# Kernel optimization log

Hardware: AMD Instinct MI355X
Metric: run time of the kernel (lower is better)

The kernel has to match this reference:

```python
import jax, jax.numpy as jnp
import numpy as np

B, H, D = 2, 16, 64
M = N = 4096
WM = WN = 64
R = 3
NEG = -10000.0


def _rand_blocks(m, n, wm, wn, r, last_idx):
    # Faithful port of bigbird_block_rand_mask (numpy RNG, seeded by caller).
    nb = m // wm
    rand = np.zeros((nb - 2, r), dtype=np.int32)
    mid = np.arange(1, n // wn - 1, dtype=np.int32)
    last = n // wn - 1
    if last_idx > 2 * wn:
        last = last_idx // wn - 1
    for i in range(1, nb - 1):
        start, end = i - 2, i
        if i == 1:
            rand[i - 1] = np.random.permutation(mid[2:last])[:r]
        elif i == 2:
            rand[i - 1] = np.random.permutation(mid[3:last])[:r]
        elif i == nb - 3 or i == nb - 2:
            rand[i - 1] = np.random.permutation(mid[:last])[:r]
        elif start > last:
            rand[i - 1] = np.random.permutation(mid[:last])[:r]
        elif end + 1 == last:
            rand[i - 1] = np.random.permutation(mid[:start])[:r]
        else:
            rand[i - 1] = np.random.permutation(np.concatenate((mid[:start], mid[end + 1:last])))[:r]
    return rand


def setup_inputs() -> dict:
    key = jax.random.key(0)
    kq, kk, kv = jax.random.split(key, 3)
    nb = M // WM
    q = jax.random.normal(kq, (B, H, M, D), jnp.float32)
    k = jax.random.normal(kk, (B, H, N, D), jnp.float32)
    v = jax.random.normal(kv, (B, H, N, D), jnp.float32)
    band_mask = jnp.ones((B, 1, nb - 4, WM, 3 * WN), jnp.float32)
    from_mask = jnp.ones((B, 1, M, 1), jnp.float32)
    to_mask = jnp.ones((B, 1, 1, N), jnp.float32)
    from_blocked_mask = jnp.ones((B, nb, WM), jnp.float32)
    to_blocked_mask = jnp.ones((B, nb, WN), jnp.float32)
    np.random.seed(0)
    ra = np.stack([_rand_blocks(M, N, WM, WN, R, 1024)[:nb - 2] for _ in range(H)], 0)
    rand_attn = jnp.asarray(np.broadcast_to(ra[None], (B, H, nb - 2, R)).copy(), jnp.int32)
    return dict(query_layer=q, key_layer=k, value_layer=v, band_mask=band_mask,
                from_mask=from_mask, to_mask=to_mask,
                from_blocked_mask=from_blocked_mask, to_blocked_mask=to_blocked_mask,
                rand_attn=rand_attn, batch_size=B, from_seq_length=M, to_seq_length=N)


def _forward(q, k, v, band_mask, from_mask, to_mask, from_blocked_mask, to_blocked_mask, rand_attn):
    b, h, m, d = q.shape
    n = k.shape[2]
    wm, wn, r = WM, WN, R
    nb = m // wm
    scale = 1.0 / np.sqrt(d)
    bq = q.reshape(b, h, nb, wm, d)
    bk = k.reshape(b, h, nb, wn, d)
    bv = v.reshape(b, h, nb, wn, d)

    # gather random key/value blocks: [b,h,nb-2,r*wn,d]
    idx = jnp.broadcast_to(rand_attn.reshape(b, h, (nb - 2) * r, 1, 1).astype(jnp.int32),
                           (b, h, (nb - 2) * r, wn, d))
    gk = jnp.take_along_axis(bk, idx, axis=2).reshape(b, h, nb - 2, r * wn, d)
    gv = jnp.take_along_axis(bv, idx, axis=2).reshape(b, h, nb - 2, r * wn, d)

    # random-block attention mask: [b,h,nb-2,wm,r*wn]
    bidx = jnp.arange(b)[:, None, None, None]
    rm = to_blocked_mask[bidx, rand_attn].reshape(b, h, nb - 2, r * wn)
    rand_mask = jnp.einsum('blq,bhlk->bhlqk', from_blocked_mask[:, 1:-1], rm)

    # --- first row-block: full attention over all keys ---
    p0 = jnp.einsum('bhqd,bhkd->bhqk', bq[:, :, 0], k) * scale + (1.0 - to_mask) * NEG
    c0 = jnp.einsum('bhqk,bhkd->bhqd', jax.nn.softmax(p0, -1), v)[:, :, None]

    # --- second row-block: blocks 0,1,2,last + random ---
    k1c = jnp.concatenate([bk[:, :, 0], bk[:, :, 1], bk[:, :, 2], bk[:, :, -1], gk[:, :, 0]], axis=2)
    v1c = jnp.concatenate([bv[:, :, 0], bv[:, :, 1], bv[:, :, 2], bv[:, :, -1], gv[:, :, 0]], axis=2)
    p1 = jnp.einsum('bhqd,bhkd->bhqk', bq[:, :, 1], k1c) * scale
    seq_pad = jnp.concatenate([to_mask[:, :, :, :3 * wn], to_mask[:, :, :, -wn:],
                               jnp.ones((b, 1, 1, r * wn), to_mask.dtype)], axis=3)
    rpad = jnp.concatenate([jnp.ones((b, h, wm, 4 * wn), rand_mask.dtype), rand_mask[:, :, 0]], axis=3)
    p1 = p1 + (1.0 - jnp.minimum(seq_pad, rpad)) * NEG
    c1 = jnp.einsum('bhqk,bhkd->bhqd', jax.nn.softmax(p1, -1), v1c)[:, :, None]

    # --- middle row-blocks: sliding window (3 blocks) + first + last + random ---
    ek = jnp.concatenate([bk[:, :, 1:-3], bk[:, :, 2:-2], bk[:, :, 3:-1]], axis=3)  # [b,h,nb-4,3wn,d]
    ev = jnp.concatenate([bv[:, :, 1:-3], bv[:, :, 2:-2], bv[:, :, 3:-1]], axis=3)
    mq = bq[:, :, 2:-2]
    inner = jnp.einsum('bhlqd,bhlkd->bhlqk', mq, ek) * scale + (1.0 - band_mask) * NEG
    randp = jnp.einsum('bhlqd,bhlkd->bhlqk', mq, gk[:, :, 1:-1]) * scale + (1.0 - rand_mask[:, :, 1:-1]) * NEG
    firstp = jnp.einsum('bhlqd,bhkd->bhlqk', mq, bk[:, :, 0]) * scale \
        + (1.0 - to_mask[:, :, :, :wn][:, :, :, None, :]) * NEG
    lastp = jnp.einsum('bhlqd,bhkd->bhlqk', mq, bk[:, :, -1]) * scale \
        + (1.0 - to_mask[:, :, :, -wn:][:, :, :, None, :]) * NEG
    band = jnp.concatenate([firstp, inner, randp, lastp], axis=-1)  # [b,h,nb-4,wm,(5+r)*wn]
    attn = jax.nn.softmax(band, -1)
    cmid = (jnp.einsum('bhlqk,bhlkd->bhlqd', attn[..., wn:4 * wn], ev)
            + jnp.einsum('bhlqk,bhlkd->bhlqd', attn[..., 4 * wn:4 * wn + r * wn], gv[:, :, 1:-1])
            + jnp.einsum('bhlqk,bhkd->bhlqd', attn[..., :wn], bv[:, :, 0])
            + jnp.einsum('bhlqk,bhkd->bhlqd', attn[..., -wn:], bv[:, :, -1]))

    # --- second-to-last row-block: blocks 0,-3,-2,-1 + random ---
    k2c = jnp.concatenate([bk[:, :, 0], bk[:, :, -3], bk[:, :, -2], bk[:, :, -1], gk[:, :, -1]], axis=2)
    v2c = jnp.concatenate([bv[:, :, 0], bv[:, :, -3], bv[:, :, -2], bv[:, :, -1], gv[:, :, -1]], axis=2)
    p2 = jnp.einsum('bhqd,bhkd->bhqk', bq[:, :, -2], k2c) * scale
    seq_pad2 = jnp.concatenate([to_mask[:, :, :, :wn], to_mask[:, :, :, -3 * wn:],
                                jnp.ones((b, 1, 1, r * wn), to_mask.dtype)], axis=3)
    rpad2 = jnp.concatenate([jnp.ones((b, h, wm, 4 * wn), rand_mask.dtype), rand_mask[:, :, -1]], axis=3)
    p2 = p2 + (1.0 - jnp.minimum(seq_pad2, rpad2)) * NEG
    c2 = jnp.einsum('bhqk,bhkd->bhqd', jax.nn.softmax(p2, -1), v2c)[:, :, None]

    # --- last row-block: full attention ---
    p3 = jnp.einsum('bhqd,bhkd->bhqk', bq[:, :, -1], k) * scale + (1.0 - to_mask) * NEG
    c3 = jnp.einsum('bhqk,bhkd->bhqd', jax.nn.softmax(p3, -1), v)[:, :, None]

    ctx = jnp.concatenate([c0, c1, cmid, c2, c3], axis=2).reshape(b, h, m, d) * from_mask
    return jnp.transpose(ctx, (0, 2, 1, 3))  # [b, m, h, d]


def reference(query_layer, key_layer, value_layer, band_mask, from_mask, to_mask,
              from_blocked_mask, to_blocked_mask, rand_attn,
              batch_size, from_seq_length, to_seq_length):
    return _forward(query_layer, key_layer, value_layer, band_mask, from_mask, to_mask,
                    from_blocked_mask, to_blocked_mask, rand_attn)
```

## Files before the change

### kernel.cpp

```cpp
#include <hip/hip_runtime.h>
#include <math.h>

constexpr int B_  = 2;
constexpr int H_  = 16;
constexpr int M_  = 4096;
constexpr int NB_ = 64;
constexpr int R_  = 3;
constexpr float LOG2E  = 1.44269504089f;
constexpr float SCALE2 = 0.125f * LOG2E;
constexpr float NEG2   = -10000.0f * LOG2E;

constexpr int PER_BH = 62 + 16;
constexpr int NWG    = B_ * H_ * PER_BH;
constexpr int PACC_OFF = 0;
constexpr int PM_OFF   = B_ * H_ * 2 * 8 * 64 * 64;
constexpr int PL_OFF   = PM_OFF + B_ * H_ * 2 * 8 * 64;
constexpr size_t KV_BYTE_OFF = (size_t)(PL_OFF + B_ * H_ * 2 * 8 * 64) * 4;
constexpr size_t KV_BYTES    = (size_t)B_ * H_ * 64 * 1024 * 16;
constexpr size_t WS_NEED     = KV_BYTE_OFF + KV_BYTES;

constexpr int PER_BH1 = 312;
constexpr int NWG1    = B_ * H_ * PER_BH1;

typedef short bf16x8 __attribute__((ext_vector_type(8)));
typedef float f32x4  __attribute__((ext_vector_type(4)));

__device__ __forceinline__ short bf16s(float x) {
    return __builtin_bit_cast(short, (__bf16)x);
}
__device__ __forceinline__ unsigned pack_bf16(float a, float b) {
    unsigned short ul = __builtin_bit_cast(unsigned short, (__bf16)a);
    unsigned short uh = __builtin_bit_cast(unsigned short, (__bf16)b);
    return (unsigned)ul | ((unsigned)uh << 16);
}

__device__ __forceinline__ int tile_kb(int e, int ch, int qb, int ra0, int ra1, int ra2, int i) {
    if (e >= 0) return ch * 8 + i;
    const int rnd = (i == 4) ? ra0 : ((i == 5) ? ra1 : ra2);
    if (qb == 1)        return (i < 3) ? i : ((i == 3) ? NB_ - 1 : rnd);
    if (qb == NB_ - 2)  return (i == 0) ? 0 : ((i < 4) ? 60 + i : rnd);
    if (i == 0) return 0;
    if (i < 4)  return qb - 2 + i;
    if (i < 7)  return rnd;
    return NB_ - 1;
}

__device__ __forceinline__ int tile_mode(int e, int qb, int i, int& boff) {
    boff = 0;
    if (e >= 0) return 0;
    if (qb == 1 || qb == NB_ - 2) return (i >= 4) ? 2 : 0;
    if (i >= 1 && i < 4) { boff = (i - 1) * 64; return 1; }
    if (i >= 4 && i < 7) return 2;
    return 0;
}

__global__ __launch_bounds__(256)
void bigbird_prep(const float* __restrict__ k, const float* __restrict__ v,
                  int4* __restrict__ wskv)
{
    __shared__ float kt[64][66];
    __shared__ float vt[64][66];
    const int g = blockIdx.x;
    const int t = threadIdx.x;
    const int row = t >> 2, cc = (t & 3) * 16;
    const float* kp = k + (size_t)g * 4096 + row * 64 + cc;
    const float* vp = v + (size_t)g * 4096 + row * 64 + cc;
    #pragma unroll
    for (int j4 = 0; j4 < 4; ++j4) {
        *(float4*)&kt[row][cc + j4 * 4] = *(const float4*)(kp + j4 * 4);
        *(float4*)&vt[row][cc + j4 * 4] = *(const float4*)(vp + j4 * 4);
    }
    __syncthreads();
    #pragma unroll
    for (int cpt = 0; cpt < 4; ++cpt) {
        const int ch = t + cpt * 256;
        const int slot = ch >> 6, lane = ch & 63;
        bf16x8 o;
        if (slot < 8) {
            const int r  = 16 * (slot >> 1) + (lane & 15);
            const int c0 = 32 * (slot & 1) + 8 * (lane >> 4);
            #pragma unroll
            for (int j = 0; j < 8; ++j) o[j] = bf16s(kt[r][c0 + j]);
        } else {
            const int s2 = slot - 8;
            const int r0 = 32 * (s2 & 1) + 8 * (lane >> 4);
            const int c  = 16 * (s2 >> 1) + (lane & 15);
            #pragma unroll
            for (int j = 0; j < 8; ++j) o[j] = bf16s(vt[r0 + j][c]);
        }
        wskv[(size_t)g * 1024 + ch] = __builtin_bit_cast(int4, o);
    }
}

__global__ __launch_bounds__(64, 3)
void bigbird_1w(const float* __restrict__ q, const int4* __restrict__ wskv,
                const float* __restrict__ band_mask, const float* __restrict__ from_mask,
                const float* __restrict__ to_mask,   const float* __restrict__ from_blocked,
                const float* __restrict__ to_blocked, const int* __restrict__ rand_attn,
                float* __restrict__ out, float* __restrict__ ws)
{
    const int wg   = (blockIdx.x & 7) * (NWG1 / 8) + (blockIdx.x >> 3);
    const int bh   = wg / PER_BH1;
    const int idx  = wg % PER_BH1;
    const int item = idx >> 2;
    const int strip= idx & 3;
    const int h    = bh % H_;
    const int b    = bh / H_;
    int qb, e = -1, ch = 0;
    if (item < 62)      { qb = item + 1; }
    else if (item < 70) { e = 0; ch = item - 62; qb = 0; }
    else                { e = 1; ch = item - 70; qb = NB_ - 1; }

    const int l  = threadIdx.x;
    const int c  = l & 15;
    const int hh = l >> 4;

    int ra0 = 0, ra1 = 0, ra2 = 0;
    int nkb;
    if (e >= 0) nkb = 8;
    else {
        const int* ra = rand_attn + ((b * H_ + h) * (NB_ - 2) + (qb - 1)) * R_;
        ra0 = ra[0]; ra1 = ra[1]; ra2 = ra[2];
        nkb = (qb == 1 || qb == NB_ - 2) ? 7 : 8;
    }

    bf16x8 qf[2];
    {
        const float* qp = q + ((size_t)bh * M_ + (size_t)qb * 64 + strip * 16 + c) * 64 + hh * 8;
        #pragma unroll
        for (int dh = 0; dh < 2; ++dh) {
            float4 a0 = *(const float4*)(qp + dh * 32);
            float4 a1 = *(const float4*)(qp + dh * 32 + 4);
            bf16x8 qv;
            qv[0] = bf16s(a0.x); qv[1] = bf16s(a0.y); qv[2] = bf16s(a0.z); qv[3] = bf16s(a0.w);
            qv[4] = bf16s(a1.x); qv[5] = bf16s(a1.y); qv[6] = bf16s(a1.z); qv[7] = bf16s(a1.w);
            qf[dh] = qv;
        }
    }

    const float fbv = from_blocked[(b * NB_ + qb) * 64 + (strip * 16 + c)];

    float mrun = -INFINITY, lrun = 0.0f;
    f32x4 O[4];
    #pragma unroll
    for (int nf = 0; nf < 4; ++nf) { O[nf][0] = 0.f; O[nf][1] = 0.f; O[nf][2] = 0.f; O[nf][3] = 0.f; }

    for (int it = 0; it < nkb; ++it) {
        const int kb = tile_kb(e, ch, qb, ra0, ra1, ra2, it);
        int boffC; const int modeC = tile_mode(e, qb, it, boffC);
        const int4* tb = wskv + (size_t)(bh * 64 + kb) * 1024;

        int4 kfr[8];
        #pragma unroll
        for (int s = 0; s < 8; ++s) kfr[s] = tb[s * 64 + l];
        int4 vfr[8];
        #pragma unroll
        for (int s = 0; s < 8; ++s) vfr[s] = tb[(8 + s) * 64 + l];

        float msk[4][4];
        if (modeC == 0) {
            const float* mp = to_mask + b * M_ + kb * 64 + 4 * hh;
            #pragma unroll
            for (int f = 0; f < 4; ++f) {
                float4 mv = *(const float4*)(mp + 16 * f);
                msk[f][0] = mv.x; msk[f][1] = mv.y; msk[f][2] = mv.z; msk[f][3] = mv.w;
            }
        } else if (modeC == 1) {
            const float* mp = band_mask + (((size_t)b * (NB_ - 4) + (qb - 2)) * 64 + (strip * 16 + c)) * 192 + boffC + 4 * hh;
            #pragma unroll
            for (int f = 0; f < 4; ++f) {
                float4 mv = *(const float4*)(mp + 16 * f);
                msk[f][0] = mv.x; msk[f][1] = mv.y; msk[f][2] = mv.z; msk[f][3] = mv.w;
            }
        } else {
            const float* mp = to_blocked + (b * NB_ + kb) * 64 + 4 * hh;
            #pragma unroll
            for (int f = 0; f < 4; ++f) {
                float4 mv = *(const float4*)(mp + 16 * f);
                msk[f][0] = fbv * mv.x; msk[f][1] = fbv * mv.y;
                msk[f][2] = fbv * mv.z; msk[f][3] = fbv * mv.w;
            }
        }

        f32x4 sf[4];
        #pragma unroll
        for (int f = 0; f < 4; ++f) { sf[f][0]=0.f; sf[f][1]=0.f; sf[f][2]=0.f; sf[f][3]=0.f; }
        __builtin_amdgcn_s_setprio(1);
        #pragma unroll
        for (int f = 0; f < 4; ++f) {
            sf[f] = __builtin_amdgcn_mfma_f32_16x16x32_bf16(
                        __builtin_bit_cast(bf16x8, kfr[f * 2 + 0]), qf[0], sf[f], 0, 0, 0);
            sf[f] = __builtin_amdgcn_mfma_f32_16x16x32_bf16(
                        __builtin_bit_cast(bf16x8, kfr[f * 2 + 1]), qf[1], sf[f], 0, 0, 0);
        }
        __builtin_amdgcn_s_setprio(0);

        float p[4][4];
        float tmax = -INFINITY;
        #pragma unroll
        for (int f = 0; f < 4; ++f) {
            #pragma unroll
            for (int r = 0; r < 4; ++r) {
                const float s = sf[f][r] * SCALE2 + (1.0f - msk[f][r]) * NEG2;
                p[f][r] = s;
                tmax = fmaxf(tmax, s);
            }
        }
        tmax = fmaxf(tmax, __shfl_xor(tmax, 16));
        tmax = fmaxf(tmax, __shfl_xor(tmax, 32));
        const float mnew = fmaxf(mrun, tmax);
        const float fs = exp2f(mrun - mnew);
        float sum = 0.0f;
        #pragma unroll
        for (int f = 0; f < 4; ++f) {
            #pragma unroll
            for (int r = 0; r < 4; ++r) { p[f][r] = exp2f(p[f][r] - mnew); sum += p[f][r]; }
        }
        sum += __shfl_xor(sum, 16);
        sum += __shfl_xor(sum, 32);
        lrun = lrun * fs + sum;
        mrun = mnew;

        const float fr0 = __shfl(fs, hh * 4 + 0);
        const float fr1 = __shfl(fs, hh * 4 + 1);
        const float fr2 = __shfl(fs, hh * 4 + 2);
        const float fr3 = __shfl(fs, hh * 4 + 3);
        #pragma unroll
        for (int nf = 0; nf < 4; ++nf) {
            O[nf][0] *= fr0; O[nf][1] *= fr1; O[nf][2] *= fr2; O[nf][3] *= fr3;
        }

        unsigned pks[4][2];
        #pragma unroll
        for (int f = 0; f < 4; ++f) {
            pks[f][0] = pack_bf16(p[f][0], p[f][1]);
            pks[f][1] = pack_bf16(p[f][2], p[f][3]);
        }
        #pragma unroll
        for (int kh = 0; kh < 2; ++kh) {
            unsigned ad[4];
            #pragma unroll
            for (int wq = 0; wq < 4; ++wq) {
                const int pos = wq >> 1, ww = wq & 1;
                const int src = c + 16 * ((2 * hh + pos) & 3);
                const unsigned x = (unsigned)__shfl((int)pks[2 * kh][ww], src);
                const unsigned y = (unsigned)__shfl((int)pks[2 * kh + 1][ww], src);
                ad[wq] = (hh & 2) ? y : x;
            }
            const uint4 adv = make_uint4(ad[0], ad[1], ad[2], ad[3]);
            const bf16x8 pa = __builtin_bit_cast(bf16x8, adv);
            __builtin_amdgcn_s_setprio(1);
            #pragma unroll
            for (int nf = 0; nf < 4; ++nf) {
                O[nf] = __builtin_amdgcn_mfma_f32_16x16x32_bf16(
                            pa, __builtin_bit_cast(bf16x8, vfr[nf * 2 + kh]), O[nf], 0, 0, 0);
            }
            __builtin_amdgcn_s_setprio(0);
        }
    }

    if (e < 0) {
        #pragma unroll
        for (int r = 0; r < 4; ++r) {
            const float lr  = __shfl(lrun, hh * 4 + r);
            const int   qg  = qb * 64 + strip * 16 + hh * 4 + r;
            const float fmv = from_mask[b * M_ + qg];
            const float scl = fmv / lr;
            float* op = out + (((size_t)b * M_ + qg) * H_ + h) * 64 + c;
            #pragma unroll
            for (int nf = 0; nf < 4; ++nf) op[nf * 16] = O[nf][r] * scl;
        }
    } else {
        const int pe = (bh * 2 + e) * 8 + ch;
        #pragma unroll
        for (int r = 0; r < 4; ++r) {
            const int qlocal = strip * 16 + hh * 4 + r;
            float* pa = ws + PACC_OFF + ((size_t)pe * 64 + qlocal) * 64 + c;
            #pragma unroll
            for (int nf = 0; nf < 4; ++nf) pa[nf * 16] = O[nf][r];
        }
        if (hh == 0) {
            ws[PM_OFF + pe * 64 + strip * 16 + c] = mrun;
            ws[PL_OFF + pe * 64 + strip * 16 + c] = lrun;
        }
    }
}

__global__ __launch_bounds__(256, 4)
void bigbird_mfma(const float* __restrict__ q,  const float* __restrict__ k,
                  const float* __restrict__ v,  const float* __restrict__ band_mask,
                  const float* __restrict__ from_mask, const float* __restrict__ to_mask,
                  const float* __restrict__ from_blocked, const float* __restrict__ to_blocked,
                  const int*   __restrict__ rand_attn,   float* __restrict__ out,
                  float* __restrict__ ws)
{
    __shared__ int4 kf[2][8][64];
    __shared__ int4 vf[2][8][64];

    const int wg  = (blockIdx.x & 7) * (NWG / 8) + (blockIdx.x >> 3);
    const int bh  = wg / PER_BH;
    const int idx = wg % PER_BH;
    const int h   = bh % H_;
    const int b   = bh / H_;
    int qb, e = -1, ch = 0;
    if (idx < 62)      { qb = idx + 1; }
    else if (idx < 70) { e = 0; ch = idx - 62; qb = 0; }
    else               { e = 1; ch = idx - 70; qb = NB_ - 1; }

    const int t  = threadIdx.x;
    const int l  = t & 63;
    const int w  = t >> 6;
    const int c  = l & 15;
    const int hh = l >> 4;

    int ra0 = 0, ra1 = 0, ra2 = 0;
    int nkb;
    if (e >= 0) nkb = 8;
    else {
        const int* ra = rand_attn + ((b * H_ + h) * (NB_ - 2) + (qb - 1)) * R_;
        ra0 = ra[0]; ra1 = ra[1]; ra2 = ra[2];
        nkb = (qb == 1 || qb == NB_ - 2) ? 7 : 8;
    }

    const int rr  = t >> 2;
    const int cc4 = t & 3;
    const float* kbase = k + ((size_t)bh * M_ + rr) * 64 + cc4 * 16;
    const int kslot = (rr >> 4) * 2 + (cc4 >> 1);
    const int kr15  = rr & 15;
    const int kg0   = (cc4 & 1) * 2;

    const int d0v  = (t & 31) * 2;
    const int oct8 = t >> 5;
    const float* vbase = v + (size_t)bh * M_ * 64 + (size_t)(oct8 * 8) * 64 + d0v;
    const int vslot = (d0v >> 4) * 2 + (oct8 >> 2);
    const int vidx  = (oct8 & 3) * 16 + (d0v & 15);

    bf16x8 qf[2];
    {
        const float* qp = q + ((size_t)bh * M_ + (size_t)qb * 64 + w * 16 + c) * 64 + hh * 8;
        #pragma unroll
        for (int dh = 0; dh < 2; ++dh) {
            float4 a0 = *(const float4*)(qp + dh * 32);
            float4 a1 = *(const float4*)(qp + dh * 32 + 4);
            bf16x8 qv;
            qv[0] = bf16s(a0.x); qv[1] = bf16s(a0.y); qv[2] = bf16s(a0.z); qv[3] = bf16s(a0.w);
            qv[4] = bf16s(a1.x); qv[5] = bf16s(a1.y); qv[6] = bf16s(a1.z); qv[7] = bf16s(a1.w);
            qf[dh] = qv;
        }
    }

    const float fbv = from_blocked[(b * NB_ + qb) * 64 + (w * 16 + c)];

    float mrun = -INFINITY, lrun = 0.0f;
    f32x4 O[4];
    #pragma unroll
    for (int nf = 0; nf < 4; ++nf) { O[nf][0] = 0.f; O[nf][1] = 0.f; O[nf][2] = 0.f; O[nf][3] = 0.f; }

    float4 kr0, kr1, kr2, kr3;
    float2 vr[8];

    {
        const int kb0 = tile_kb(e, ch, qb, ra0, ra1, ra2, 0);
        const float4* kp4 = (const float4*)(kbase + (size_t)kb0 * 4096);
        kr0 = kp4[0]; kr1 = kp4[1]; kr2 = kp4[2]; kr3 = kp4[3];
        const float* vp = vbase + (size_t)kb0 * 4096;
        #pragma unroll
        for (int j = 0; j < 8; ++j) vr[j] = *(const float2*)(vp + j * 64);

        float kfl[16];
        kfl[0]=kr0.x; kfl[1]=kr0.y; kfl[2]=kr0.z; kfl[3]=kr0.w;
        kfl[4]=kr1.x; kfl[5]=kr1.y; kfl[6]=kr1.z; kfl[7]=kr1.w;
        kfl[8]=kr2.x; kfl[9]=kr2.y; kfl[10]=kr2.z; kfl[11]=kr2.w;
        kfl[12]=kr3.x; kfl[13]=kr3.y; kfl[14]=kr3.z; kfl[15]=kr3.w;
        bf16x8 o0, o1;
        #pragma unroll
        for (int j = 0; j < 8; ++j) { o0[j] = bf16s(kfl[j]); o1[j] = bf16s(kfl[8 + j]); }
        kf[0][kslot][kg0 * 16 + kr15]       = __builtin_bit_cast(int4, o0);
        kf[0][kslot][(kg0 + 1) * 16 + kr15] = __builtin_bit_cast(int4, o1);

        bf16x8 va, vb2;
        #pragma unroll
        for (int j = 0; j < 8; ++j) { va[j] = bf16s(vr[j].x); vb2[j] = bf16s(vr[j].y); }
        vf[0][vslot][vidx]     = __builtin_bit_cast(int4, va);
        vf[0][vslot][vidx + 1] = __builtin_bit_cast(int4, vb2);

        if (1 < nkb) {
            const int kb1 = tile_kb(e, ch, qb, ra0, ra1, ra2, 1);
            const float4* kn4 = (const float4*)(kbase + (size_t)kb1 * 4096);
            kr0 = kn4[0]; kr1 = kn4[1]; kr2 = kn4[2]; kr3 = kn4[3];
            const float* vn = vbase + (size_t)kb1 * 4096;
            #pragma unroll
            for (int j = 0; j < 8; ++j) vr[j] = *(const float2*)(vn + j * 64);
        }
    }
    __syncthreads();

    for (int it = 0; it < nkb; ++it) {
        const int cur = it & 1;
        const int kb = tile_kb(e, ch, qb, ra0, ra1, ra2, it);
        int boffC; const int modeC = tile_mode(e, qb, it, boffC);

        f32x4 sf[4];
        #pragma unroll
        for (int f = 0; f < 4; ++f) { sf[f][0]=0.f; sf[f][1]=0.f; sf[f][2]=0.f; sf[f][3]=0.f; }
        __builtin_amdgcn_s_setprio(1);
        #pragma unroll
        for (int f = 0; f < 4; ++f) {
            sf[f] = __builtin_amdgcn_mfma_f32_16x16x32_bf16(
                        __builtin_bit_cast(bf16x8, kf[cur][f * 2 + 0][l]), qf[0], sf[f], 0, 0, 0);
            sf[f] = __builtin_amdgcn_mfma_f32_16x16x32_bf16(
                        __builtin_bit_cast(bf16x8, kf[cur][f * 2 + 1][l]), qf[1], sf[f], 0, 0, 0);
        }
        __builtin_amdgcn_s_setprio(0);

        if (it + 1 < nkb) {
            const int nxt = cur ^ 1;
            float kfl[16];
            kfl[0]=kr0.x; kfl[1]=kr0.y; kfl[2]=kr0.z; kfl[3]=kr0.w;
            kfl[4]=kr1.x; kfl[5]=kr1.y; kfl[6]=kr1.z; kfl[7]=kr1.w;
            kfl[8]=kr2.x; kfl[9]=kr2.y; kfl[10]=kr2.z; kfl[11]=kr2.w;
            kfl[12]=kr3.x; kfl[13]=kr3.y; kfl[14]=kr3.z; kfl[15]=kr3.w;
            bf16x8 o0, o1;
            #pragma unroll
            for (int j = 0; j < 8; ++j) { o0[j] = bf16s(kfl[j]); o1[j] = bf16s(kfl[8 + j]); }
            kf[nxt][kslot][kg0 * 16 + kr15]       = __builtin_bit_cast(int4, o0);
            kf[nxt][kslot][(kg0 + 1) * 16 + kr15] = __builtin_bit_cast(int4, o1);

            bf16x8 va, vb2;
            #pragma unroll
            for (int j = 0; j < 8; ++j) { va[j] = bf16s(vr[j].x); vb2[j] = bf16s(vr[j].y); }
            vf[nxt][vslot][vidx]     = __builtin_bit_cast(int4, va);
            vf[nxt][vslot][vidx + 1] = __builtin_bit_cast(int4, vb2);
        }

        float msk[4][4];
        if (modeC == 0) {
            const float* mp = to_mask + b * M_ + kb * 64 + 4 * hh;
            #pragma unroll
            for (int f = 0; f < 4; ++f) {
                float4 mv = *(const float4*)(mp + 16 * f);
                msk[f][0] = mv.x; msk[f][1] = mv.y; msk[f][2] = mv.z; msk[f][3] = mv.w;
            }
        } else if (modeC == 1) {
            const float* mp = band_mask + (((size_t)b * (NB_ - 4) + (qb - 2)) * 64 + (w * 16 + c)) * 192 + boffC + 4 * hh;
            #pragma unroll
            for (int f = 0; f < 4; ++f) {
                float4 mv = *(const float4*)(mp + 16 * f);
                msk[f][0] = mv.x; msk[f][1] = mv.y; msk[f][2] = mv.z; msk[f][3] = mv.w;
            }
        } else {
            const float* mp = to_blocked + (b * NB_ + kb) * 64 + 4 * hh;
            #pragma unroll
            for (int f = 0; f < 4; ++f) {
                float4 mv = *(const float4*)(mp + 16 * f);
                msk[f][0] = fbv * mv.x; msk[f][1] = fbv * mv.y;
                msk[f][2] = fbv * mv.z; msk[f][3] = fbv * mv.w;
            }
        }

        if (it + 2 < nkb) {
            const int kb2 = tile_kb(e, ch, qb, ra0, ra1, ra2, it + 2);
            const float4* kp4 = (const float4*)(kbase + (size_t)kb2 * 4096);
            kr0 = kp4[0]; kr1 = kp4[1]; kr2 = kp4[2]; kr3 = kp4[3];
            const float* vp = vbase + (size_t)kb2 * 4096;
            #pragma unroll
            for (int j = 0; j < 8; ++j) vr[j] = *(const float2*)(vp + j * 64);
        }

        float p[4][4];
        float tmax = -INFINITY;
        #pragma unroll
        for (int f = 0; f < 4; ++f) {
            #pragma unroll
            for (int r = 0; r < 4; ++r) {
                const float s = sf[f][r] * SCALE2 + (1.0f - msk[f][r]) * NEG2;
                p[f][r] = s;
                tmax = fmaxf(tmax, s);
            }
        }
        tmax = fmaxf(tmax, __shfl_xor(tmax, 16));
        tmax = fmaxf(tmax, __shfl_xor(tmax, 32));
        const float mnew = fmaxf(mrun, tmax);
        const float fs = exp2f(mrun - mnew);
        float sum = 0.0f;
        #pragma unroll
        for (int f = 0; f < 4; ++f) {
            #pragma unroll
            for (int r = 0; r < 4; ++r) { p[f][r] = exp2f(p[f][r] - mnew); sum += p[f][r]; }
        }
        sum += __shfl_xor(sum, 16);
        sum += __shfl_xor(sum, 32);
        lrun = lrun * fs + sum;
        mrun = mnew;

        const float fr0 = __shfl(fs, hh * 4 + 0);
        const float fr1 = __shfl(fs, hh * 4 + 1);
        const float fr2 = __shfl(fs, hh * 4 + 2);
        const float fr3 = __shfl(fs, hh * 4 + 3);
        #pragma unroll
        for (int nf = 0; nf < 4; ++nf) {
            O[nf][0] *= fr0; O[nf][1] *= fr1; O[nf][2] *= fr2; O[nf][3] *= fr3;
        }

        unsigned pks[4][2];
        #pragma unroll
        for (int f = 0; f < 4; ++f) {
            pks[f][0] = pack_bf16(p[f][0], p[f][1]);
            pks[f][1] = pack_bf16(p[f][2], p[f][3]);
        }
        #pragma unroll
        for (int kh = 0; kh < 2; ++kh) {
            unsigned ad[4];
            #pragma unroll
            for (int wq = 0; wq < 4; ++wq) {
                const int pos = wq >> 1, ww = wq & 1;
                const int src = c + 16 * ((2 * hh + pos) & 3);
                const unsigned x = (unsigned)__shfl((int)pks[2 * kh][ww], src);
                const unsigned y = (unsigned)__shfl((int)pks[2 * kh + 1][ww], src);
                ad[wq] = (hh & 2) ? y : x;
            }
            const uint4 adv = make_uint4(ad[0], ad[1], ad[2], ad[3]);
            const bf16x8 pa = __builtin_bit_cast(bf16x8, adv);
            __builtin_amdgcn_s_setprio(1);
            #pragma unroll
            for (int nf = 0; nf < 4; ++nf) {
                O[nf] = __builtin_amdgcn_mfma_f32_16x16x32_bf16(
                            pa, __builtin_bit_cast(bf16x8, vf[cur][nf * 2 + kh][l]), O[nf], 0, 0, 0);
            }
            __builtin_amdgcn_s_setprio(0);
        }

        __syncthreads();
    }

    if (e < 0) {
        #pragma unroll
        for (int r = 0; r < 4; ++r) {
            const float lr  = __shfl(lrun, hh * 4 + r);
            const int   qg  = qb * 64 + w * 16 + hh * 4 + r;
            const float fmv = from_mask[b * M_ + qg];
            const float scl = fmv / lr;
            float* op = out + (((size_t)b * M_ + qg) * H_ + h) * 64 + c;
            #pragma unroll
            for (int nf = 0; nf < 4; ++nf) op[nf * 16] = O[nf][r] * scl;
        }
    } else {
        const int pe = (bh * 2 + e) * 8 + ch;
        #pragma unroll
        for (int r = 0; r < 4; ++r) {
            const int qlocal = w * 16 + hh * 4 + r;
            float* pa = ws + PACC_OFF + ((size_t)pe * 64 + qlocal) * 64 + c;
            #pragma unroll
            for (int nf = 0; nf < 4; ++nf) pa[nf * 16] = O[nf][r];
        }
        if (hh == 0) {
            ws[PM_OFF + pe * 64 + w * 16 + c] = mrun;
            ws[PL_OFF + pe * 64 + w * 16 + c] = lrun;
        }
    }
}

__global__ __launch_bounds__(256)
void bigbird_combine(const float* __restrict__ ws, const float* __restrict__ from_mask,
                     float* __restrict__ out)
{
    const int g  = blockIdx.x;
    const int e  = g & 1;
    const int bh = g >> 1;
    const int h  = bh % H_;
    const int b  = bh / H_;
    const int qb = e ? NB_ - 1 : 0;

    const int t  = threadIdx.x;
    const int r  = t >> 2;
    const int dq = (t & 3) * 16;

    float mc[8], lc[8];
    float m = -INFINITY;
    #pragma unroll
    for (int c = 0; c < 8; ++c) {
        mc[c] = ws[PM_OFF + (g * 8 + c) * 64 + r];
        lc[c] = ws[PL_OFF + (g * 8 + c) * 64 + r];
        m = fmaxf(m, mc[c]);
    }
    float l = 0.0f;
    float acc[16];
    #pragma unroll
    for (int j = 0; j < 16; ++j) acc[j] = 0.0f;
    #pragma unroll
    for (int c = 0; c < 8; ++c) {
        const float sc = exp2f(mc[c] - m);
        l += lc[c] * sc;
        const float4* pa = (const float4*)(ws + PACC_OFF + ((size_t)(g * 8 + c) * 64 + r) * 64 + dq);
        #pragma unroll
        for (int j4 = 0; j4 < 4; ++j4) {
            float4 av = pa[j4];
            acc[j4 * 4 + 0] += sc * av.x;
            acc[j4 * 4 + 1] += sc * av.y;
            acc[j4 * 4 + 2] += sc * av.z;
            acc[j4 * 4 + 3] += sc * av.w;
        }
    }
    const float fm = from_mask[b * M_ + qb * 64 + r];
    const float s  = fm / l;
    float* op = out + (((size_t)b * M_ + qb * 64 + r) * H_ + h) * 64 + dq;
    #pragma unroll
    for (int j4 = 0; j4 < 4; ++j4) {
        float4 o;
        o.x = acc[j4 * 4 + 0] * s; o.y = acc[j4 * 4 + 1] * s;
        o.z = acc[j4 * 4 + 2] * s; o.w = acc[j4 * 4 + 3] * s;
        *(float4*)(op + j4 * 4) = o;
    }
}

extern "C" void kernel_launch(void* const* d_in, const int* in_sizes, int n_in,
                              void* d_out, int out_size, void* d_ws, size_t ws_size,
                              hipStream_t stream) {
    const float* q  = (const float*)d_in[0];
    const float* k  = (const float*)d_in[1];
    const float* v  = (const float*)d_in[2];
    const float* bm = (const float*)d_in[3];
    const float* fm = (const float*)d_in[4];
    const float* tm = (const float*)d_in[5];
    const float* fb = (const float*)d_in[6];
    const float* tb = (const float*)d_in[7];
    const int*   ra = (const int*)d_in[8];
    float* o  = (float*)d_out;
    float* ws = (float*)d_ws;

    if (ws_size >= WS_NEED) {
        int4* wskv = (int4*)((char*)d_ws + KV_BYTE_OFF);
        hipLaunchKernelGGL(bigbird_prep, dim3(B_ * H_ * 64), dim3(256), 0, stream,
                           k, v, wskv);
        hipLaunchKernelGGL(bigbird_1w, dim3(NWG1), dim3(64), 0, stream,
                           q, wskv, bm, fm, tm, fb, tb, ra, o, ws);
    } else {
        hipLaunchKernelGGL(bigbird_mfma, dim3(NWG), dim3(256), 0, stream,
                           q, k, v, bm, fm, tm, fb, tb, ra, o, ws);
    }
    hipLaunchKernelGGL(bigbird_combine, dim3(B_ * H_ * 2), dim3(256), 0, stream,
                       ws, fm, o);
}
```

Before: 97.94 us.

## Software-pipeline K/V tile and mask loads one iteration ahead

Prefetches the next key tile after the QK MFMAs, the next mask after the softmax, and the next value tile after the PV MFMAs, all into registers, so global-load latency overlaps with compute of the current tile. The per-mode mask branches are collapsed into one pointer lambda plus a multiplier. This overwrites the current kfr/vfr in place once they are consumed. It adds control flow and may raise register pressure, which could lower occupancy.

```diff
diff --git a/kernel.cpp b/kernel.cpp
--- a/kernel.cpp
+++ b/kernel.cpp
@@ -124,6 +124,12 @@
         nkb = (qb == 1 || qb == NB_ - 2) ? 7 : 8;
     }
 
+    auto mask_ptr = [&](int kb, int mode, int boff) -> const float* {
+        if (mode == 0) return to_mask + b * M_ + kb * 64 + 4 * hh;
+        if (mode == 1) return band_mask + (((size_t)b * (NB_ - 4) + (qb - 2)) * 64 + (strip * 16 + c)) * 192 + boff + 4 * hh;
+        return to_blocked + (b * NB_ + kb) * 64 + 4 * hh;
+    };
+
     bf16x8 qf[2];
     {
         const float* qp = q + ((size_t)bh * M_ + (size_t)qb * 64 + strip * 16 + c) * 64 + hh * 8;
@@ -145,41 +151,30 @@
     #pragma unroll
     for (int nf = 0; nf < 4; ++nf) { O[nf][0] = 0.f; O[nf][1] = 0.f; O[nf][2] = 0.f; O[nf][3] = 0.f; }
 
+    int4 kfr[8], vfr[8];
+    float4 mpf[4];
+    int modeC;
+    {
+        const int kb0 = tile_kb(e, ch, qb, ra0, ra1, ra2, 0);
+        int bo0; modeC = tile_mode(e, qb, 0, bo0);
+        const int4* tb = wskv + (size_t)(bh * 64 + kb0) * 1024;
+        #pragma unroll
+        for (int s = 0; s < 8; ++s) kfr[s] = tb[s * 64 + l];
+        const float* mp = mask_ptr(kb0, modeC, bo0);
+        #pragma unroll
+        for (int f = 0; f < 4; ++f) mpf[f] = *(const float4*)(mp + 16 * f);
+        #pragma unroll
+        for (int s = 0; s < 8; ++s) vfr[s] = tb[(8 + s) * 64 + l];
+    }
+
     for (int it = 0; it < nkb; ++it) {
-        const int kb = tile_kb(e, ch, qb, ra0, ra1, ra2, it);
-        int boffC; const int modeC = tile_mode(e, qb, it, boffC);
-        const int4* tb = wskv + (size_t)(bh * 64 + kb) * 1024;
-
-        int4 kfr[8];
-        #pragma unroll
-        for (int s = 0; s < 8; ++s) kfr[s] = tb[s * 64 + l];
-        int4 vfr[8];
-        #pragma unroll
-        for (int s = 0; s < 8; ++s) vfr[s] = tb[(8 + s) * 64 + l];
-
-        float msk[4][4];
-        if (modeC == 0) {
-            const float* mp = to_mask + b * M_ + kb * 64 + 4 * hh;
-            #pragma unroll
-            for (int f = 0; f < 4; ++f) {
-                float4 mv = *(const float4*)(mp + 16 * f);
-                msk[f][0] = mv.x; msk[f][1] = mv.y; msk[f][2] = mv.z; msk[f][3] = mv.w;
-            }
-        } else if (modeC == 1) {
-            const float* mp = band_mask + (((size_t)b * (NB_ - 4) + (qb - 2)) * 64 + (strip * 16 + c)) * 192 + boffC + 4 * hh;
-            #pragma unroll
-            for (int f = 0; f < 4; ++f) {
-                float4 mv = *(const float4*)(mp + 16 * f);
-                msk[f][0] = mv.x; msk[f][1] = mv.y; msk[f][2] = mv.z; msk[f][3] = mv.w;
-            }
-        } else {
-            const float* mp = to_blocked + (b * NB_ + kb) * 64 + 4 * hh;
-            #pragma unroll
-            for (int f = 0; f < 4; ++f) {
-                float4 mv = *(const float4*)(mp + 16 * f);
-                msk[f][0] = fbv * mv.x; msk[f][1] = fbv * mv.y;
-                msk[f][2] = fbv * mv.z; msk[f][3] = fbv * mv.w;
-            }
+        const bool hasN = (it + 1 < nkb);
+        int kbN = 0, boN = 0, modeN = 0;
+        const int4* tbN = wskv;
+        if (hasN) {
+            kbN  = tile_kb(e, ch, qb, ra0, ra1, ra2, it + 1);
+            modeN = tile_mode(e, qb, it + 1, boN);
+            tbN  = wskv + (size_t)(bh * 64 + kbN) * 1024;
         }
 
         f32x4 sf[4];
@@ -195,16 +190,23 @@
         }
         __builtin_amdgcn_s_setprio(0);
 
+        if (hasN) {
+            #pragma unroll
+            for (int s = 0; s < 8; ++s) kfr[s] = tbN[s * 64 + l];
+        }
+
+        const float ms = (modeC == 2) ? fbv : 1.0f;
         float p[4][4];
         float tmax = -INFINITY;
         #pragma unroll
         for (int f = 0; f < 4; ++f) {
-            #pragma unroll
-            for (int r = 0; r < 4; ++r) {
-                const float s = sf[f][r] * SCALE2 + (1.0f - msk[f][r]) * NEG2;
-                p[f][r] = s;
-                tmax = fmaxf(tmax, s);
-            }
+            const float m0 = ms * mpf[f].x, m1 = ms * mpf[f].y;
+            const float m2 = ms * mpf[f].z, m3 = ms * mpf[f].w;
+            p[f][0] = sf[f][0] * SCALE2 + (1.0f - m0) * NEG2;
+            p[f][1] = sf[f][1] * SCALE2 + (1.0f - m1) * NEG2;
+            p[f][2] = sf[f][2] * SCALE2 + (1.0f - m2) * NEG2;
+            p[f][3] = sf[f][3] * SCALE2 + (1.0f - m3) * NEG2;
+            tmax = fmaxf(tmax, fmaxf(fmaxf(p[f][0], p[f][1]), fmaxf(p[f][2], p[f][3])));
         }
         tmax = fmaxf(tmax, __shfl_xor(tmax, 16));
         tmax = fmaxf(tmax, __shfl_xor(tmax, 32));
@@ -220,6 +222,12 @@
         sum += __shfl_xor(sum, 32);
         lrun = lrun * fs + sum;
         mrun = mnew;
+
+        if (hasN) {
+            const float* mp = mask_ptr(kbN, modeN, boN);
+            #pragma unroll
+            for (int f = 0; f < 4; ++f) mpf[f] = *(const float4*)(mp + 16 * f);
+        }
 
         const float fr0 = __shfl(fs, hh * 4 + 0);
         const float fr1 = __shfl(fs, hh * 4 + 1);
@@ -257,6 +265,13 @@
             }
             __builtin_amdgcn_s_setprio(0);
         }
+
+        if (hasN) {
+            #pragma unroll
+            for (int s = 0; s < 8; ++s) vfr[s] = tbN[(8 + s) * 64 + l];
+        }
+
+        modeC = modeN;
     }
 
     if (e < 0) {
```

After: 95.42 us. 1.03x faster.

## Split single-wave KV loop into two interleaved online-softmax streams

Applied to the files above, without the earlier changes.

The single-wave kernel now processes KV tiles in two independent streams (first half and second half of the tile list), each with its own running max, sum and output accumulator, and merges them at the end. The goal is more instruction-level parallelism: loads and MFMAs of one stream can overlap the softmax dependency chain of the other. In exchange it roughly doubles register pressure, so launch bounds drop from 3 to 2 waves per SIMD, which lowers occupancy. Mask loads are also unified behind a pointer helper, with a multiplier applied for the blocked mode.

```diff
diff --git a/kernel.cpp b/kernel.cpp
--- a/kernel.cpp
+++ b/kernel.cpp
@@ -92,7 +92,7 @@
     }
 }
 
-__global__ __launch_bounds__(64, 3)
+__global__ __launch_bounds__(64, 2)
 void bigbird_1w(const float* __restrict__ q, const int4* __restrict__ wskv,
                 const float* __restrict__ band_mask, const float* __restrict__ from_mask,
                 const float* __restrict__ to_mask,   const float* __restrict__ from_blocked,
@@ -123,6 +123,13 @@
         ra0 = ra[0]; ra1 = ra[1]; ra2 = ra[2];
         nkb = (qb == 1 || qb == NB_ - 2) ? 7 : 8;
     }
+    const int halfA = 4;
+
+    auto mask_ptr = [&](int kb, int mode, int boff) -> const float* {
+        if (mode == 0) return to_mask + b * M_ + kb * 64 + 4 * hh;
+        if (mode == 1) return band_mask + (((size_t)b * (NB_ - 4) + (qb - 2)) * 64 + (strip * 16 + c)) * 192 + boff + 4 * hh;
+        return to_blocked + (b * NB_ + kb) * 64 + 4 * hh;
+    };
 
     bf16x8 qf[2];
     {
@@ -140,129 +147,231 @@
 
     const float fbv = from_blocked[(b * NB_ + qb) * 64 + (strip * 16 + c)];
 
-    float mrun = -INFINITY, lrun = 0.0f;
+    float mA = -INFINITY, lA = 0.0f, mB = -INFINITY, lB = 0.0f;
+    f32x4 OA[4], OB[4];
+    #pragma unroll
+    for (int nf = 0; nf < 4; ++nf) {
+        OA[nf][0]=0.f; OA[nf][1]=0.f; OA[nf][2]=0.f; OA[nf][3]=0.f;
+        OB[nf][0]=0.f; OB[nf][1]=0.f; OB[nf][2]=0.f; OB[nf][3]=0.f;
+    }
+
+    for (int it = 0; it < halfA; ++it) {
+        const int  iA   = it;
+        const int  iB   = halfA + it;
+        const bool hasB = (iB < nkb);
+
+        const int kbA = tile_kb(e, ch, qb, ra0, ra1, ra2, iA);
+        int boA; const int moA = tile_mode(e, qb, iA, boA);
+        const int4* tbA = wskv + (size_t)(bh * 64 + kbA) * 1024;
+        int kbB = 0, boB = 0, moB = 0; const int4* tbB = wskv;
+        if (hasB) {
+            kbB = tile_kb(e, ch, qb, ra0, ra1, ra2, iB);
+            moB = tile_mode(e, qb, iB, boB);
+            tbB = wskv + (size_t)(bh * 64 + kbB) * 1024;
+        }
+
+        int4 kfrA[8], kfrB[8];
+        #pragma unroll
+        for (int s = 0; s < 8; ++s) kfrA[s] = tbA[s * 64 + l];
+        if (hasB) {
+            #pragma unroll
+            for (int s = 0; s < 8; ++s) kfrB[s] = tbB[s * 64 + l];
+        }
+        float4 mpfA[4], mpfB[4];
+        {
+            const float* mp = mask_ptr(kbA, moA, boA);
+            #pragma unroll
+            for (int f = 0; f < 4; ++f) mpfA[f] = *(const float4*)(mp + 16 * f);
+        }
+        if (hasB) {
+            const float* mp = mask_ptr(kbB, moB, boB);
+            #pragma unroll
+            for (int f = 0; f < 4; ++f) mpfB[f] = *(const float4*)(mp + 16 * f);
+        }
+
+        f32x4 sfA[4], sfB[4];
+        #pragma unroll
+        for (int f = 0; f < 4; ++f) { sfA[f][0]=0.f; sfA[f][1]=0.f; sfA[f][2]=0.f; sfA[f][3]=0.f; }
+        __builtin_amdgcn_s_setprio(1);
+        #pragma unroll
+        for (int f = 0; f < 4; ++f) {
+            sfA[f] = __builtin_amdgcn_mfma_f32_16x16x32_bf16(
+                         __builtin_bit_cast(bf16x8, kfrA[f * 2 + 0]), qf[0], sfA[f], 0, 0, 0);
+            sfA[f] = __builtin_amdgcn_mfma_f32_16x16x32_bf16(
+                         __builtin_bit_cast(bf16x8, kfrA[f * 2 + 1]), qf[1], sfA[f], 0, 0, 0);
+        }
+        __builtin_amdgcn_s_setprio(0);
+        if (hasB) {
+            #pragma unroll
+            for (int f = 0; f < 4; ++f) { sfB[f][0]=0.f; sfB[f][1]=0.f; sfB[f][2]=0.f; sfB[f][3]=0.f; }
+            __builtin_amdgcn_s_setprio(1);
+            #pragma unroll
+            for (int f = 0; f < 4; ++f) {
+                sfB[f] = __builtin_amdgcn_mfma_f32_16x16x32_bf16(
+                             __builtin_bit_cast(bf16x8, kfrB[f * 2 + 0]), qf[0], sfB[f], 0, 0, 0);
+                sfB[f] = __builtin_amdgcn_mfma_f32_16x16x32_bf16(
+                             __builtin_bit_cast(bf16x8, kfrB[f * 2 + 1]), qf[1], sfB[f], 0, 0, 0);
+            }
+            __builtin_amdgcn_s_setprio(0);
+        }
+
+        int4 vfrA[8], vfrB[8];
+        #pragma unroll
+        for (int s = 0; s < 8; ++s) vfrA[s] = tbA[(8 + s) * 64 + l];
+        if (hasB) {
+            #pragma unroll
+            for (int s = 0; s < 8; ++s) vfrB[s] = tbB[(8 + s) * 64 + l];
+        }
+
+        {
+            const float ms = (moA == 2) ? fbv : 1.0f;
+            float p[4][4];
+            float tmax = -INFINITY;
+            #pragma unroll
+            for (int f = 0; f < 4; ++f) {
+                p[f][0] = sfA[f][0] * SCALE2 + (1.0f - ms * mpfA[f].x) * NEG2;
+                p[f][1] = sfA[f][1] * SCALE2 + (1.0f - ms * mpfA[f].y) * NEG2;
+                p[f][2] = sfA[f][2] * SCALE2 + (1.0f - ms * mpfA[f].z) * NEG2;
+                p[f][3] = sfA[f][3] * SCALE2 + (1.0f - ms * mpfA[f].w) * NEG2;
+                tmax = fmaxf(tmax, fmaxf(fmaxf(p[f][0], p[f][1]), fmaxf(p[f][2], p[f][3])));
+            }
+            tmax = fmaxf(tmax, __shfl_xor(tmax, 16));
+            tmax = fmaxf(tmax, __shfl_xor(tmax, 32));
+            const float mnew = fmaxf(mA, tmax);
+            const float fs = exp2f(mA - mnew);
+            float sum = 0.0f;
+            #pragma unroll
+            for (int f = 0; f < 4; ++f) {
+                #pragma unroll
+                for (int r = 0; r < 4; ++r) { p[f][r] = exp2f(p[f][r] - mnew); sum += p[f][r]; }
+            }
+            sum += __shfl_xor(sum, 16);
+            sum += __shfl_xor(sum, 32);
+            lA = lA * fs + sum;
+            mA = mnew;
+
+            const float fr0 = __shfl(fs, hh * 4 + 0);
+            const float fr1 = __shfl(fs, hh * 4 + 1);
+            const float fr2 = __shfl(fs, hh * 4 + 2);
+            const float fr3 = __shfl(fs, hh * 4 + 3);
+            #pragma unroll
+            for (int nf = 0; nf < 4; ++nf) {
+                OA[nf][0] *= fr0; OA[nf][1] *= fr1; OA[nf][2] *= fr2; OA[nf][3] *= fr3;
+            }
+
+            unsigned pks[4][2];
+            #pragma unroll
+            for (int f = 0; f < 4; ++f) {
+                pks[f][0] = pack_bf16(p[f][0], p[f][1]);
+                pks[f][1] = pack_bf16(p[f][2], p[f][3]);
+            }
+            #pragma unroll
+            for (int kh = 0; kh < 2; ++kh) {
+                unsigned ad[4];
+                #pragma unroll
+                for (int wq = 0; wq < 4; ++wq) {
+                    const int pos = wq >> 1, ww = wq & 1;
+                    const int src = c + 16 * ((2 * hh + pos) & 3);
+                    const unsigned x = (unsigned)__shfl((int)pks[2 * kh][ww], src);
+                    const unsigned y = (unsigned)__shfl((int)pks[2 * kh + 1][ww], src);
+                    ad[wq] = (hh & 2) ? y : x;
+                }
+                const uint4 adv = make_uint4(ad[0], ad[1], ad[2], ad[3]);
+                const bf16x8 pa = __builtin_bit_cast(bf16x8, adv);
+                __builtin_amdgcn_s_setprio(1);
+                #pragma unroll
+                for (int nf = 0; nf < 4; ++nf) {
+                    OA[nf] = __builtin_amdgcn_mfma_f32_16x16x32_bf16(
+                                 pa, __builtin_bit_cast(bf16x8, vfrA[nf * 2 + kh]), OA[nf], 0, 0, 0);
+                }
+                __builtin_amdgcn_s_setprio(0);
+            }
+        }
+
+        if (hasB) {
+            const float ms = (moB == 2) ? fbv : 1.0f;
+            float p[4][4];
+            float tmax = -INFINITY;
+            #pragma unroll
+            for (int f = 0; f < 4; ++f) {
+                p[f][0] = sfB[f][0] * SCALE2 + (1.0f - ms * mpfB[f].x) * NEG2;
+                p[f][1] = sfB[f][1] * SCALE2 + (1.0f - ms * mpfB[f].y) * NEG2;
+                p[f][2] = sfB[f][2] * SCALE2 + (1.0f - ms * mpfB[f].z) * NEG2;
+                p[f][3] = sfB[f][3] * SCALE2 + (1.0f - ms * mpfB[f].w) * NEG2;
+                tmax = fmaxf(tmax, fmaxf(fmaxf(p[f][0], p[f][1]), fmaxf(p[f][2], p[f][3])));
+            }
+            tmax = fmaxf(tmax, __shfl_xor(tmax, 16));
+            tmax = fmaxf(tmax, __shfl_xor(tmax, 32));
+            const float mnew = fmaxf(mB, tmax);
+            const float fs = exp2f(mB - mnew);
+            float sum = 0.0f;
+            #pragma unroll
+            for (int f = 0; f < 4; ++f) {
+                #pragma unroll
+                for (int r = 0; r < 4; ++r) { p[f][r] = exp2f(p[f][r] - mnew); sum += p[f][r]; }
+            }
+            sum += __shfl_xor(sum, 16);
+            sum += __shfl_xor(sum, 32);
+            lB = lB * fs + sum;
+            mB = mnew;
+
+            const float fr0 = __shfl(fs, hh * 4 + 0);
+            const float fr1 = __shfl(fs, hh * 4 + 1);
+            const float fr2 = __shfl(fs, hh * 4 + 2);
+            const float fr3 = __shfl(fs, hh * 4 + 3);
+            #pragma unroll
+            for (int nf = 0; nf < 4; ++nf) {
+                OB[nf][0] *= fr0; OB[nf][1] *= fr1; OB[nf][2] *= fr2; OB[nf][3] *= fr3;
+            }
+
+            unsigned pks[4][2];
+            #pragma unroll
+            for (int f = 0; f < 4; ++f) {
+                pks[f][0] = pack_bf16(p[f][0], p[f][1]);
+                pks[f][1] = pack_bf16(p[f][2], p[f][3]);
+            }
+            #pragma unroll
+            for (int kh = 0; kh < 2; ++kh) {
+                unsigned ad[4];
+                #pragma unroll
+                for (int wq = 0; wq < 4; ++wq) {
+                    const int pos = wq >> 1, ww = wq & 1;
+                    const int src = c + 16 * ((2 * hh + pos) & 3);
+                    const unsigned x = (unsigned)__shfl((int)pks[2 * kh][ww], src);
+                    const unsigned y = (unsigned)__shfl((int)pks[2 * kh + 1][ww], src);
+                    ad[wq] = (hh & 2) ? y : x;
+                }
+                const uint4 adv = make_uint4(ad[0], ad[1], ad[2], ad[3]);
+                const bf16x8 pa = __builtin_bit_cast(bf16x8, adv);
+                __builtin_amdgcn_s_setprio(1);
+                #pragma unroll
+                for (int nf = 0; nf < 4; ++nf) {
+                    OB[nf] = __builtin_amdgcn_mfma_f32_16x16x32_bf16(
+                                 pa, __builtin_bit_cast(bf16x8, vfrB[nf * 2 + kh]), OB[nf], 0, 0, 0);
+                }
+                __builtin_amdgcn_s_setprio(0);
+            }
+        }
+    }
+
+    const float mM  = fmaxf(mA, mB);
+    const float sAq = exp2f(mA - mM);
+    const float sBq = exp2f(mB - mM);
+    const float lM  = lA * sAq + lB * sBq;
+
     f32x4 O[4];
     #pragma unroll
-    for (int nf = 0; nf < 4; ++nf) { O[nf][0] = 0.f; O[nf][1] = 0.f; O[nf][2] = 0.f; O[nf][3] = 0.f; }
-
-    for (int it = 0; it < nkb; ++it) {
-        const int kb = tile_kb(e, ch, qb, ra0, ra1, ra2, it);
-        int boffC; const int modeC = tile_mode(e, qb, it, boffC);
-        const int4* tb = wskv + (size_t)(bh * 64 + kb) * 1024;
-
-        int4 kfr[8];
-        #pragma unroll
-        for (int s = 0; s < 8; ++s) kfr[s] = tb[s * 64 + l];
-        int4 vfr[8];
-        #pragma unroll
-        for (int s = 0; s < 8; ++s) vfr[s] = tb[(8 + s) * 64 + l];
-
-        float msk[4][4];
-        if (modeC == 0) {
-            const float* mp = to_mask + b * M_ + kb * 64 + 4 * hh;
-            #pragma unroll
-            for (int f = 0; f < 4; ++f) {
-                float4 mv = *(const float4*)(mp + 16 * f);
-                msk[f][0] = mv.x; msk[f][1] = mv.y; msk[f][2] = mv.z; msk[f][3] = mv.w;
-            }
-        } else if (modeC == 1) {
-            const float* mp = band_mask + (((size_t)b * (NB_ - 4) + (qb - 2)) * 64 + (strip * 16 + c)) * 192 + boffC + 4 * hh;
-            #pragma unroll
-            for (int f = 0; f < 4; ++f) {
-                float4 mv = *(const float4*)(mp + 16 * f);
-                msk[f][0] = mv.x; msk[f][1] = mv.y; msk[f][2] = mv.z; msk[f][3] = mv.w;
-            }
-        } else {
-            const float* mp = to_blocked + (b * NB_ + kb) * 64 + 4 * hh;
-            #pragma unroll
-            for (int f = 0; f < 4; ++f) {
-                float4 mv = *(const float4*)(mp + 16 * f);
-                msk[f][0] = fbv * mv.x; msk[f][1] = fbv * mv.y;
-                msk[f][2] = fbv * mv.z; msk[f][3] = fbv * mv.w;
-            }
-        }
-
-        f32x4 sf[4];
-        #pragma unroll
-        for (int f = 0; f < 4; ++f) { sf[f][0]=0.f; sf[f][1]=0.f; sf[f][2]=0.f; sf[f][3]=0.f; }
-        __builtin_amdgcn_s_setprio(1);
-        #pragma unroll
-        for (int f = 0; f < 4; ++f) {
-            sf[f] = __builtin_amdgcn_mfma_f32_16x16x32_bf16(
-                        __builtin_bit_cast(bf16x8, kfr[f * 2 + 0]), qf[0], sf[f], 0, 0, 0);
-            sf[f] = __builtin_amdgcn_mfma_f32_16x16x32_bf16(
-                        __builtin_bit_cast(bf16x8, kfr[f * 2 + 1]), qf[1], sf[f], 0, 0, 0);
-        }
-        __builtin_amdgcn_s_setprio(0);
-
-        float p[4][4];
-        float tmax = -INFINITY;
-        #pragma unroll
-        for (int f = 0; f < 4; ++f) {
-            #pragma unroll
-            for (int r = 0; r < 4; ++r) {
-                const float s = sf[f][r] * SCALE2 + (1.0f - msk[f][r]) * NEG2;
-                p[f][r] = s;
-                tmax = fmaxf(tmax, s);
-            }
-        }
-        tmax = fmaxf(tmax, __shfl_xor(tmax, 16));
-        tmax = fmaxf(tmax, __shfl_xor(tmax, 32));
-        const float mnew = fmaxf(mrun, tmax);
-        const float fs = exp2f(mrun - mnew);
-        float sum = 0.0f;
-        #pragma unroll
-        for (int f = 0; f < 4; ++f) {
-            #pragma unroll
-            for (int r = 0; r < 4; ++r) { p[f][r] = exp2f(p[f][r] - mnew); sum += p[f][r]; }
-        }
-        sum += __shfl_xor(sum, 16);
-        sum += __shfl_xor(sum, 32);
-        lrun = lrun * fs + sum;
-        mrun = mnew;
-
-        const float fr0 = __shfl(fs, hh * 4 + 0);
-        const float fr1 = __shfl(fs, hh * 4 + 1);
-        const float fr2 = __shfl(fs, hh * 4 + 2);
-        const float fr3 = __shfl(fs, hh * 4 + 3);
-        #pragma unroll
-        for (int nf = 0; nf < 4; ++nf) {
-            O[nf][0] *= fr0; O[nf][1] *= fr1; O[nf][2] *= fr2; O[nf][3] *= fr3;
-        }
-
-        unsigned pks[4][2];
-        #pragma unroll
-        for (int f = 0; f < 4; ++f) {
-            pks[f][0] = pack_bf16(p[f][0], p[f][1]);
-            pks[f][1] = pack_bf16(p[f][2], p[f][3]);
-        }
-        #pragma unroll
-        for (int kh = 0; kh < 2; ++kh) {
-            unsigned ad[4];
-            #pragma unroll
-            for (int wq = 0; wq < 4; ++wq) {
-                const int pos = wq >> 1, ww = wq & 1;
-                const int src = c + 16 * ((2 * hh + pos) & 3);
-                const unsigned x = (unsigned)__shfl((int)pks[2 * kh][ww], src);
-                const unsigned y = (unsigned)__shfl((int)pks[2 * kh + 1][ww], src);
-                ad[wq] = (hh & 2) ? y : x;
-            }
-            const uint4 adv = make_uint4(ad[0], ad[1], ad[2], ad[3]);
-            const bf16x8 pa = __builtin_bit_cast(bf16x8, adv);
-            __builtin_amdgcn_s_setprio(1);
-            #pragma unroll
-            for (int nf = 0; nf < 4; ++nf) {
-                O[nf] = __builtin_amdgcn_mfma_f32_16x16x32_bf16(
-                            pa, __builtin_bit_cast(bf16x8, vfr[nf * 2 + kh]), O[nf], 0, 0, 0);
-            }
-            __builtin_amdgcn_s_setprio(0);
-        }
+    for (int r = 0; r < 4; ++r) {
+        const float fAr = __shfl(sAq, hh * 4 + r);
+        const float fBr = __shfl(sBq, hh * 4 + r);
+        #pragma unroll
+        for (int nf = 0; nf < 4; ++nf) O[nf][r] = OA[nf][r] * fAr + OB[nf][r] * fBr;
     }
 
     if (e < 0) {
         #pragma unroll
         for (int r = 0; r < 4; ++r) {
-            const float lr  = __shfl(lrun, hh * 4 + r);
+            const float lr  = __shfl(lM, hh * 4 + r);
             const int   qg  = qb * 64 + strip * 16 + hh * 4 + r;
             const float fmv = from_mask[b * M_ + qg];
             const float scl = fmv / lr;
@@ -280,8 +389,8 @@
             for (int nf = 0; nf < 4; ++nf) pa[nf * 16] = O[nf][r];
         }
         if (hh == 0) {
-            ws[PM_OFF + pe * 64 + strip * 16 + c] = mrun;
-            ws[PL_OFF + pe * 64 + strip * 16 + c] = lrun;
+            ws[PM_OFF + pe * 64 + strip * 16 + c] = mM;
+            ws[PL_OFF + pe * 64 + strip * 16 + c] = lM;
         }
     }
 }
```

Measured after the change: 104.4 us. +6.6%, slower.
